# Kernel optimization log

Measured on AMD Instinct MI355X. Metric: run time of the kernel, lower is better.

The kernel has to match this reference:

```python
import jax, jax.numpy as jnp
import numpy as np

NUM_Q = 8
CODEBOOK_SIZE = 1024
DIM = 512
TEMP = 0.1


def _conv1d(x, w, b):
    # x: [B, C_in, T], w: [C_out, C_in, 3], padding 'same' (pad 1 each side)
    y = jax.lax.conv_general_dilated(
        x, w, window_strides=(1,), padding=((1, 1),),
        dimension_numbers=("NCH", "OIH", "NCH"))
    return y + b[None, :, None]


def _gelu(x):
    return jax.nn.gelu(x, approximate=False)  # torch default GELU is exact erf


def setup_inputs() -> dict:
    key = jax.random.key(0)
    ks = jax.random.split(key, 10)
    B, T = 8, 2048
    s = 0.05
    return {
        "x": jax.random.normal(ks[0], (B, T, 100), jnp.float32),
        "enc_w1": jax.random.normal(ks[1], (256, 100, 3), jnp.float32) * s,
        "enc_b1": jnp.zeros((256,), jnp.float32),
        "enc_w2": jax.random.normal(ks[2], (512, 256, 3), jnp.float32) * s,
        "enc_b2": jnp.zeros((512,), jnp.float32),
        "codebook": jax.random.normal(ks[3], (CODEBOOK_SIZE, DIM), jnp.float32),
        "dec_w1": jax.random.normal(ks[4], (256, 512, 3), jnp.float32) * s,
        "dec_b1": jnp.zeros((256,), jnp.float32),
        "dec_w2": jax.random.normal(ks[5], (100, 256, 3), jnp.float32) * s,
        "dec_b2": jnp.zeros((100,), jnp.float32),
    }


def reference(x, enc_w1, enc_b1, enc_w2, enc_b2, codebook,
              dec_w1, dec_b1, dec_w2, dec_b2):
    # ---- encoder: Conv1d(100->256)+GELU, Conv1d(256->512)+GELU ----
    h = jnp.transpose(x, (0, 2, 1))                      # [B, 100, T]
    h = _gelu(_conv1d(h, enc_w1, enc_b1))
    h = _gelu(_conv1d(h, enc_w2, enc_b2))
    z = jnp.transpose(h, (0, 2, 1))                      # [B, T, 512]

    # ---- residual VQ, 8 stages, shared euclidean codebook, stochastic sampling ----
    gkey = jax.random.key(42)
    c_sq = jnp.sum(codebook * codebook, axis=-1)         # [K]
    residual = z
    q_out = jnp.zeros_like(z)
    losses = []
    for i in range(NUM_Q):
        # negative squared euclidean distance [B, T, K]
        dist = -(jnp.sum(residual * residual, axis=-1, keepdims=True)
                 - 2.0 * jnp.einsum("btd,kd->btk", residual, codebook)
                 + c_sq)
        gumbel = jax.random.gumbel(jax.random.fold_in(gkey, i), dist.shape, dist.dtype)
        idx = jnp.argmax(dist / TEMP + gumbel, axis=-1)  # [B, T]
        q = codebook[idx]                                # gather [B, T, 512]
        # commitment loss (commitment_weight = 1.0)
        losses.append(jnp.mean((jax.lax.stop_gradient(q) - residual) ** 2))
        # straight-through quantize
        q_st = residual + jax.lax.stop_gradient(q - residual)
        q_out = q_out + q_st
        residual = residual - jax.lax.stop_gradient(q)
    commit_loss = jnp.mean(jnp.stack(losses))

    # ---- decoder: Conv1d(512->256)+GELU, Conv1d(256->100)+GELU ----
    h = jnp.transpose(q_out, (0, 2, 1))                  # [B, 512, T]
    h = _gelu(_conv1d(h, dec_w1, dec_b1))
    h = _gelu(_conv1d(h, dec_w2, dec_b2))
    y = jnp.transpose(h, (0, 2, 1))                      # [B, T, 100]

    return jnp.mean((x - y) ** 2) + commit_loss
```

## Files before the change

kernel.cpp:

```cpp
#include <hip/hip_runtime.h>
#include <cstdint>

namespace {

constexpr int kT = 2048;
constexpr int kTok = 16384;
constexpr int kD = 512;
constexpr int kK = 1024;

typedef __attribute__((ext_vector_type(8))) short short8;
typedef __attribute__((ext_vector_type(4))) float f32x4;

__device__ __forceinline__ float bf2f(uint16_t u) {
  union { uint32_t i; float f; } c; c.i = ((uint32_t)u) << 16; return c.f;
}
__device__ __forceinline__ uint16_t f2bf(float x) {
  union { float f; uint32_t i; } c; c.f = x;
  uint32_t lsb = (c.i >> 16) & 1u;
  return (uint16_t)((c.i + 0x7FFFu + lsb) >> 16);
}
__device__ __forceinline__ float gelu_f(float v) {
  return 0.5f * v * (1.0f + erff(v * 0.70710678118654752440f));
}
__device__ __forceinline__ uint32_t rotl32(uint32_t x, int r) {
  return (x << r) | (x >> (32 - r));
}

__device__ __forceinline__ void tf2x32(uint32_t k0, uint32_t k1,
                                       uint32_t x0, uint32_t x1,
                                       uint32_t& o0, uint32_t& o1) {
  const uint32_t k2 = k0 ^ k1 ^ 0x1BD11BDAu;
  x0 += k0; x1 += k1;
#define TF_R(r) { x0 += x1; x1 = rotl32(x1, (r)); x1 ^= x0; }
  TF_R(13) TF_R(15) TF_R(26) TF_R(6)
  x0 += k1; x1 += k2 + 1u;
  TF_R(17) TF_R(29) TF_R(16) TF_R(24)
  x0 += k2; x1 += k0 + 2u;
  TF_R(13) TF_R(15) TF_R(26) TF_R(6)
  x0 += k0; x1 += k1 + 3u;
  TF_R(17) TF_R(29) TF_R(16) TF_R(24)
  x0 += k1; x1 += k2 + 4u;
  TF_R(13) TF_R(15) TF_R(26) TF_R(6)
  x0 += k2; x1 += k0 + 5u;
#undef TF_R
  o0 = x0; o1 = x1;
}

__device__ __forceinline__ float gumbel_bits(uint32_t bits) {
  float f = __uint_as_float((bits >> 9) | 0x3f800000u) - 1.0f;
  const float tiny = 1.17549435e-38f;
  float u = fmaxf(tiny, f + tiny);
  return -__logf(-__logf(u));
}

__device__ __forceinline__ uint32_t pk_fp8x4(float f0, float f1, float f2, float f3) {
  int v = __builtin_amdgcn_cvt_pk_fp8_f32(f0, f1, 0, 0);
  v = __builtin_amdgcn_cvt_pk_fp8_f32(f2, f3, v, 1);
  return (uint32_t)v;
}

__global__ __launch_bounds__(256) void detect_kernel(const uint32_t* __restrict__ w,
                                                     uint32_t* __restrict__ flag) {
  __shared__ int red[256];
  int c = 0;
#pragma unroll
  for (int j = 0; j < 16; ++j) {
    uint32_t v = w[threadIdx.x * 16 + j];
    uint32_t e0 = (v >> 7) & 0xFFu;
    c += (e0 >= 100u && e0 <= 130u) ? 1 : 0;
  }
  red[threadIdx.x] = c;
  __syncthreads();
  for (int st = 128; st > 0; st >>= 1) {
    if (threadIdx.x < st) red[threadIdx.x] += red[threadIdx.x + st];
    __syncthreads();
  }
  if (threadIdx.x == 0) flag[0] = (red[0] > 2048) ? 1u : 0u;
}

__device__ __forceinline__ float load_flag(const void* src, size_t i, uint32_t fl) {
  return fl ? bf2f(((const uint16_t*)src)[i]) : ((const float*)src)[i];
}

__global__ __launch_bounds__(256) void prep_kernel(
    const void* x, const void* w1, const void* b1, const void* w2, const void* b2,
    const void* w3, const void* b3, const void* w4, const void* b4,
    uint16_t* __restrict__ xbf,
    uint16_t* __restrict__ W1, uint16_t* __restrict__ W2,
    uint16_t* __restrict__ W3, uint16_t* __restrict__ W4,
    float* __restrict__ eb1, float* __restrict__ eb2,
    float* __restrict__ db1, float* __restrict__ db2,
    const uint32_t* __restrict__ flag) {
  int gi = blockIdx.x * 256 + threadIdx.x;
  uint32_t fl = flag[0];
  if (gi < 2097152) {
    int tok = gi >> 7, ci = gi & 127;
    uint16_t v = 0;
    if (ci < 100) v = f2bf(load_flag(x, (size_t)tok * 100 + ci, fl));
    xbf[gi] = v;
    return;
  }
  int i = gi - 2097152;
  if (i < 98304) {
    int tap = i / 32768, rem = i % 32768;
    int co = rem >> 7, ci = rem & 127;
    uint16_t v = 0;
    if (ci < 100) v = f2bf(load_flag(w1, ((size_t)co * 100 + ci) * 3 + tap, fl));
    W1[i] = v;
  } else if (i < 491520) {
    int li = i - 98304;
    int tap = li / 131072, rem = li % 131072;
    int co = rem >> 8, ci = rem & 255;
    W2[li] = f2bf(load_flag(w2, ((size_t)co * 256 + ci) * 3 + tap, fl));
  } else if (i < 884736) {
    int li = i - 491520;
    int tap = li / 131072, rem = li % 131072;
    int co = rem >> 9, ci = rem & 511;
    W3[li] = f2bf(load_flag(w3, ((size_t)co * 512 + ci) * 3 + tap, fl));
  } else if (i < 983040) {
    int li = i - 884736;
    int tap = li / 32768, rem = li % 32768;
    int co = rem >> 8, ci = rem & 255;
    uint16_t v = 0;
    if (co < 100) v = f2bf(load_flag(w4, ((size_t)co * 256 + ci) * 3 + tap, fl));
    W4[li] = v;
  } else if (i < 983296) {
    eb1[i - 983040] = load_flag(b1, i - 983040, fl);
  } else if (i < 983808) {
    eb2[i - 983296] = load_flag(b2, i - 983296, fl);
  } else if (i < 984064) {
    db1[i - 983808] = load_flag(b3, i - 983808, fl);
  } else if (i < 984164) {
    db2[i - 984064] = load_flag(b4, i - 984064, fl);
  }
}

__global__ __launch_bounds__(512) void cb_prep_kernel(
    const void* __restrict__ src, float* __restrict__ cbf,
    uint8_t* __restrict__ cb8, float* __restrict__ c_sq,
    const uint32_t* __restrict__ flag) {
  __shared__ float red[8];
  const int row = blockIdx.x, t = threadIdx.x;
  const size_t i = (size_t)row * 512 + t;
  float f;
  if (flag[0]) f = bf2f(((const uint16_t*)src)[i]);
  else         f = ((const float*)src)[i];
  cbf[i] = f;
  {
    int g = t >> 6;
    int rem = t & 63;
    int half = rem >> 5;
    int quad = (rem & 31) >> 3;
    int j = t & 7;
    int off = g * 64 + quad * 16 + half * 8 + j;
    cb8[(size_t)row * 512 + off] =
        (uint8_t)(__builtin_amdgcn_cvt_pk_fp8_f32(f, f, 0, 0) & 0xFF);
  }
  float s = f * f;
  for (int off = 32; off > 0; off >>= 1) s += __shfl_down(s, off, 64);
  if ((t & 63) == 0) red[t >> 6] = s;
  __syncthreads();
  if (t == 0) {
    float tot = 0.f;
#pragma unroll
    for (int j = 0; j < 8; ++j) tot += red[j];
    c_sq[row] = tot;
  }
}

__global__ __launch_bounds__(512, 2) void gram_kernel(
    const float* __restrict__ cbf, float* __restrict__ gram) {
  constexpr int AST = 520;
  __shared__ uint16_t Ab[32 * AST];
  const int tid = threadIdx.x;
  const int w = tid >> 6;
  const int lane = tid & 63;
  const int quad = lane >> 4;
  const int col = lane & 15;
  const int bi = blockIdx.x >> 1;
  const int jb = blockIdx.x & 1;

  for (int m = tid; m < 32 * 128; m += 512) {
    int r = m >> 7, c4 = (m & 127) * 4;
    float4 v = *(const float4*)(cbf + (size_t)(bi * 32 + r) * 512 + c4);
    union { uint16_t u[4]; uint2 q; } o;
    o.u[0] = f2bf(v.x); o.u[1] = f2bf(v.y);
    o.u[2] = f2bf(v.z); o.u[3] = f2bf(v.w);
    *(uint2*)(Ab + r * AST + c4) = o.q;
  }
  __syncthreads();

  f32x4 acc[2][4];
#pragma unroll
  for (int mt = 0; mt < 2; ++mt)
#pragma unroll
    for (int nt = 0; nt < 4; ++nt) acc[mt][nt] = (f32x4){0.f, 0.f, 0.f, 0.f};

#pragma unroll 1
  for (int g = 0; g < 16; ++g) {
    short8 af0 = *(const short8*)(Ab + (size_t)col * AST + g * 32 + quad * 8);
    short8 af1 = *(const short8*)(Ab + (size_t)(16 + col) * AST + g * 32 + quad * 8);
#pragma unroll
    for (int nt = 0; nt < 4; ++nt) {
      const int j = jb * 512 + w * 64 + nt * 16 + col;
      const float* bp = cbf + (size_t)j * 512 + g * 32 + quad * 8;
      float4 b0 = *(const float4*)bp;
      float4 b1 = *(const float4*)(bp + 4);
      union { uint16_t u[8]; short8 s; } bf;
      bf.u[0] = f2bf(b0.x); bf.u[1] = f2bf(b0.y);
      bf.u[2] = f2bf(b0.z); bf.u[3] = f2bf(b0.w);
      bf.u[4] = f2bf(b1.x); bf.u[5] = f2bf(b1.y);
      bf.u[6] = f2bf(b1.z); bf.u[7] = f2bf(b1.w);
      acc[0][nt] = __builtin_amdgcn_mfma_f32_16x16x32_bf16(af0, bf.s, acc[0][nt], 0, 0, 0);
      acc[1][nt] = __builtin_amdgcn_mfma_f32_16x16x32_bf16(af1, bf.s, acc[1][nt], 0, 0, 0);
    }
  }
#pragma unroll
  for (int mt = 0; mt < 2; ++mt)
#pragma unroll
    for (int nt = 0; nt < 4; ++nt)
#pragma unroll
      for (int rg = 0; rg < 4; ++rg)
        gram[(size_t)(bi * 32 + mt * 16 + quad * 4 + rg) * 1024 +
             jb * 512 + w * 64 + nt * 16 + col] = acc[mt][nt][rg];
}

template <int TOK, int CIP, int COP, int CO_REAL, int OMODE>
__global__ __launch_bounds__(256, 2) void conv_mfma_kernel(
    const uint16_t* __restrict__ A, const uint16_t* __restrict__ W,
    const float* __restrict__ bias, uint16_t* __restrict__ outb,
    const void* __restrict__ xraw, const uint32_t* __restrict__ flag,
    float* __restrict__ partial) {
  constexpr int MT = TOK / 16;
  constexpr int AST = CIP + 8;
  __shared__ uint16_t As[(TOK + 2) * AST];
  __shared__ uint16_t Bs[128 * 72];
  __shared__ float red[256];

  const int tid = threadIdx.x;
  const int w = tid >> 6;
  const int lane = tid & 63;
  const int quad = lane >> 4;
  const int col = lane & 15;
  const int tok0 = blockIdx.x * TOK;
  const int t0 = tok0 & (kT - 1);

  constexpr int AV = (TOK + 2) * (CIP / 8);
  for (int m = tid; m < AV; m += 256) {
    int r = m / (CIP / 8), c8 = m % (CIP / 8);
    bool valid = !((r == 0 && t0 == 0) || (r == TOK + 1 && t0 == kT - TOK));
    uint4 v = {0, 0, 0, 0};
    if (valid) v = *(const uint4*)(A + (size_t)(tok0 - 1 + r) * CIP + c8 * 8);
    *(uint4*)(As + r * AST + c8 * 8) = v;
  }

  float part = 0.f;
#pragma unroll 1
  for (int chunk = 0; chunk < COP / 128; ++chunk) {
    f32x4 acc[MT][2];
#pragma unroll
    for (int mt = 0; mt < MT; ++mt)
#pragma unroll
      for (int nt = 0; nt < 2; ++nt) acc[mt][nt] = (f32x4){0.f, 0.f, 0.f, 0.f};

#pragma unroll 1
    for (int tap = 0; tap < 3; ++tap) {
#pragma unroll 1
      for (int kt = 0; kt < CIP / 64; ++kt) {
        __syncthreads();
#pragma unroll
        for (int it = 0; it < 4; ++it) {
          int m = it * 256 + tid;
          int rr = m >> 3, c8 = m & 7;
          *(uint4*)(Bs + rr * 72 + c8 * 8) =
              *(const uint4*)(W + ((size_t)tap * COP + chunk * 128 + rr) * CIP + kt * 64 + c8 * 8);
        }
        __syncthreads();
#pragma unroll
        for (int kk = 0; kk < 2; ++kk) {
          short8 bf0 = *(const short8*)(Bs + (w * 32 + col) * 72 + kk * 32 + quad * 8);
          short8 bf1 = *(const short8*)(Bs + (w * 32 + 16 + col) * 72 + kk * 32 + quad * 8);
#pragma unroll
          for (int mt = 0; mt < MT; ++mt) {
            short8 af = *(const short8*)(As + (mt * 16 + col + tap) * AST + kt * 64 + kk * 32 + quad * 8);
            acc[mt][0] = __builtin_amdgcn_mfma_f32_16x16x32_bf16(af, bf0, acc[mt][0], 0, 0, 0);
            acc[mt][1] = __builtin_amdgcn_mfma_f32_16x16x32_bf16(af, bf1, acc[mt][1], 0, 0, 0);
          }
        }
      }
    }
#pragma unroll
    for (int nt = 0; nt < 2; ++nt) {
      const int co = chunk * 128 + w * 32 + nt * 16 + col;
      const float bv = (OMODE == 1 && co >= CO_REAL) ? 0.f : bias[co];
#pragma unroll
      for (int mt = 0; mt < MT; ++mt) {
#pragma unroll
        for (int rg = 0; rg < 4; ++rg) {
          const int token = tok0 + mt * 16 + quad * 4 + rg;
          float g = gelu_f(acc[mt][nt][rg] + bv);
          if constexpr (OMODE == 0) {
            outb[(size_t)token * CO_REAL + co] = f2bf(g);
          } else {
            if (co < CO_REAL) {
              float xv = load_flag(xraw, (size_t)token * CO_REAL + co, flag[0]);
              float d = xv - g;
              part += d * d;
            }
          }
        }
      }
    }
  }
  if constexpr (OMODE == 1) {
    red[tid] = part;
    __syncthreads();
    for (int st = 128; st > 0; st >>= 1) {
      if (tid < st) red[tid] += red[tid + st];
      __syncthreads();
    }
    if (tid == 0) partial[blockIdx.x] = red[0];
  }
}

__global__ __launch_bounds__(512, 4) void vq_fused_kernel(
    const uint16_t* __restrict__ z,
    uint16_t* __restrict__ Aout,
    const uint8_t* __restrict__ cb8, const float* __restrict__ cbf,
    const float* __restrict__ csqG, const float* __restrict__ gram,
    float* __restrict__ cp) {
  constexpr int AST8 = 528;
  constexpr int AST16 = 520;
  __shared__ uint8_t  As8[32 * AST8];
  __shared__ uint16_t As16[32 * AST16];
  __shared__ float csqS[1024];
  __shared__ float dmaxW[32 * 8];
  __shared__ float thrS[32];
  __shared__ float wredV[32 * 8];
  __shared__ int   wredI[32 * 8];
  __shared__ int   idxS[32];
  __shared__ float credW[8];

  const int tid = threadIdx.x;
  const int w = tid >> 6;
  const int lane = tid & 63;
  const int quad = lane >> 4;
  const int col = lane & 15;
  const int blk = blockIdx.x;
  const int tokA = blk * 16;

  if (tid < 256) ((f32x4*)csqS)[tid] = ((const f32x4*)csqG)[tid];

#pragma unroll
  for (int it = 0; it < 4; ++it) {
    int m = it * 512 + tid;
    int r = m >> 6, c8 = m & 63;
    int tk = (r < 16) ? (tokA + r) : (8192 + tokA + r - 16);
    uint4 v = *(const uint4*)(z + (size_t)tk * 512 + c8 * 8);
    *(uint4*)(As16 + r * AST16 + c8 * 8) = v;
    const uint32_t* vp = (const uint32_t*)&v;
    float f[8];
#pragma unroll
    for (int q = 0; q < 4; ++q) {
      f[q * 2]     = bf2f((uint16_t)(vp[q] & 0xFFFFu));
      f[q * 2 + 1] = bf2f((uint16_t)(vp[q] >> 16));
    }
    uint2 pk;
    pk.x = pk_fp8x4(f[0], f[1], f[2], f[3]);
    pk.y = pk_fp8x4(f[4], f[5], f[6], f[7]);
    int ks = c8 >> 2, qd = c8 & 3;
    int off = (ks >> 1) * 64 + qd * 16 + (ks & 1) * 8;
    *(uint2*)(As8 + r * AST8 + off) = pk;
  }
  __syncthreads();

  const uint8_t* bb8 = cb8 + (size_t)(w * 128 + col) * 512 + (size_t)quad * 16;
  const int lr = tid >> 4;
  const int utok = (lr < 16) ? (tokA + lr) : (8192 + tokA + lr - 16);
  uint16_t* arow = As16 + lr * AST16;

  f32x4 acc[2][8];
#pragma unroll
  for (int mt = 0; mt < 2; ++mt)
#pragma unroll
    for (int nt = 0; nt < 8; ++nt) acc[mt][nt] = (f32x4){0.f, 0.f, 0.f, 0.f};

#pragma unroll 1
  for (int stage = 0; stage < 8; ++stage) {
    uint32_t key0, key1;
    tf2x32(0u, 42u, 0u, (uint32_t)stage, key0, key1);

    if (stage == 0) {
#pragma unroll 1
      for (int g = 0; g < 8; ++g) {
        ulong2 av0 = *(const ulong2*)(As8 + (size_t)(col) * AST8 + g * 64 + quad * 16);
        ulong2 av1 = *(const ulong2*)(As8 + (size_t)(16 + col) * AST8 + g * 64 + quad * 16);
#pragma unroll
        for (int nh = 0; nh < 2; ++nh) {
          ulong2 bfr[4];
#pragma unroll
          for (int j = 0; j < 4; ++j)
            bfr[j] = *(const ulong2*)(bb8 + (size_t)(nh * 4 + j) * 8192 + g * 64);
#pragma unroll
          for (int j = 0; j < 4; ++j) {
            acc[0][nh * 4 + j] = __builtin_amdgcn_mfma_f32_16x16x32_fp8_fp8(
                (long)av0.x, (long)bfr[j].x, acc[0][nh * 4 + j], 0, 0, 0);
            acc[0][nh * 4 + j] = __builtin_amdgcn_mfma_f32_16x16x32_fp8_fp8(
                (long)av0.y, (long)bfr[j].y, acc[0][nh * 4 + j], 0, 0, 0);
            acc[1][nh * 4 + j] = __builtin_amdgcn_mfma_f32_16x16x32_fp8_fp8(
                (long)av1.x, (long)bfr[j].x, acc[1][nh * 4 + j], 0, 0, 0);
            acc[1][nh * 4 + j] = __builtin_amdgcn_mfma_f32_16x16x32_fp8_fp8(
                (long)av1.y, (long)bfr[j].y, acc[1][nh * 4 + j], 0, 0, 0);
          }
        }
      }
    }

    float dmx[2][4];
#pragma unroll
    for (int mt = 0; mt < 2; ++mt)
#pragma unroll
      for (int rg = 0; rg < 4; ++rg) dmx[mt][rg] = -INFINITY;
#pragma unroll
    for (int nt = 0; nt < 8; ++nt) {
      const int code = w * 128 + nt * 16 + col;
      const float csqv = csqS[code];
#pragma unroll
      for (int mt = 0; mt < 2; ++mt)
#pragma unroll
        for (int rg = 0; rg < 4; ++rg)
          dmx[mt][rg] = fmaxf(dmx[mt][rg], acc[mt][nt][rg] * 2.f - csqv);
    }
#pragma unroll
    for (int mt = 0; mt < 2; ++mt)
#pragma unroll
      for (int rg = 0; rg < 4; ++rg) {
        float v = dmx[mt][rg];
#pragma unroll
        for (int m = 8; m >= 1; m >>= 1) v = fmaxf(v, __shfl_xor(v, m));
        if (col == 0) dmaxW[(mt * 16 + quad * 4 + rg) * 8 + w] = v;
      }
    __syncthreads();
    if (tid < 32) {
      float v = dmaxW[tid * 8];
#pragma unroll
      for (int j = 1; j < 8; ++j) v = fmaxf(v, dmaxW[tid * 8 + j]);
      thrS[tid] = v - 2.2f;
    }
    __syncthreads();

    float thr[2][4];
#pragma unroll
    for (int mt = 0; mt < 2; ++mt)
#pragma unroll
      for (int rg = 0; rg < 4; ++rg) thr[mt][rg] = thrS[mt * 16 + quad * 4 + rg];

    float bestV[2][4];
    int bestI[2][4];
#pragma unroll
    for (int mt = 0; mt < 2; ++mt)
#pragma unroll
      for (int rg = 0; rg < 4; ++rg) { bestV[mt][rg] = -INFINITY; bestI[mt][rg] = 0; }

#pragma unroll
    for (int nt = 0; nt < 8; ++nt) {
      const int code = w * 128 + nt * 16 + col;
      const float csqv = csqS[code];
#pragma unroll
      for (int rg = 0; rg < 4; ++rg) {
        float d0 = acc[0][nt][rg] * 2.f - csqv;
        float d1 = acc[1][nt][rg] * 2.f - csqv;
        bool c0 = d0 >= thr[0][rg];
        bool c1 = d1 >= thr[1][rg];
        if (c0 || c1) {
          const int row0 = quad * 4 + rg;
          const uint32_t n = (uint32_t)(tokA + row0) * 1024u + (uint32_t)code;
          uint32_t o0, o1;
          tf2x32(key0, key1, n, n + 8388608u, o0, o1);
          if (c0) {
            float s0 = d0 * 10.f + gumbel_bits(o0);
            if (s0 > bestV[0][rg]) { bestV[0][rg] = s0; bestI[0][rg] = code; }
          }
          if (c1) {
            float s1 = d1 * 10.f + gumbel_bits(o1);
            if (s1 > bestV[1][rg]) { bestV[1][rg] = s1; bestI[1][rg] = code; }
          }
        }
      }
    }

#pragma unroll
    for (int mt = 0; mt < 2; ++mt)
#pragma unroll
      for (int rg = 0; rg < 4; ++rg) {
        float v = bestV[mt][rg];
        int i = bestI[mt][rg];
#pragma unroll
        for (int m = 8; m >= 1; m >>= 1) {
          float vo = __shfl_xor(v, m);
          int io = __shfl_xor(i, m);
          if (vo > v || (vo == v && io < i)) { v = vo; i = io; }
        }
        if (col == 0) {
          const int row = mt * 16 + quad * 4 + rg;
          wredV[row * 8 + w] = v;
          wredI[row * 8 + w] = i;
        }
      }
    __syncthreads();
    if (tid < 32) {
      float v = wredV[tid * 8];
      int i = wredI[tid * 8];
#pragma unroll
      for (int j = 1; j < 8; ++j) {
        float vo = wredV[tid * 8 + j];
        int io = wredI[tid * 8 + j];
        if (vo > v || (vo == v && io < i)) { v = vo; i = io; }
      }
      idxS[tid] = i;
    }
    __syncthreads();

    const int code = idxS[lr];
    const float* qrow = cbf + (size_t)code * 512;
    float s = 0.f;
#pragma unroll 1
    for (int it = 0; it < 8; ++it) {
      const int d = (tid & 15) * 4 + it * 64;
      float4 q = *(const float4*)(qrow + d);
      uint2 rp = *(const uint2*)(arow + d);
      union { uint16_t u[4]; uint2 v; } ri, ro;
      ri.v = rp;
      float r0 = bf2f(ri.u[0]), r1 = bf2f(ri.u[1]);
      float r2 = bf2f(ri.u[2]), r3 = bf2f(ri.u[3]);
      float d0 = q.x - r0, d1 = q.y - r1, d2 = q.z - r2, d3 = q.w - r3;
      s += d0 * d0 + d1 * d1 + d2 * d2 + d3 * d3;
      ro.u[0] = f2bf(r0 - q.x); ro.u[1] = f2bf(r1 - q.y);
      ro.u[2] = f2bf(r2 - q.z); ro.u[3] = f2bf(r3 - q.w);
      if (stage == 7) {
        uint2 zp = *(const uint2*)(z + (size_t)utok * 512 + d);
        union { uint16_t u[4]; uint2 v; } zi, od;
        zi.v = zp;
        od.u[0] = f2bf(bf2f(zi.u[0]) - bf2f(ro.u[0]));
        od.u[1] = f2bf(bf2f(zi.u[1]) - bf2f(ro.u[1]));
        od.u[2] = f2bf(bf2f(zi.u[2]) - bf2f(ro.u[2]));
        od.u[3] = f2bf(bf2f(zi.u[3]) - bf2f(ro.u[3]));
        *(uint2*)(Aout + (size_t)utok * 512 + d) = od.v;
      } else {
        *(uint2*)(arow + d) = ro.v;
      }
    }

    if (stage < 7) {
#define DGRP(MT, RG) { \
      const float* gp_ = gram + (size_t)idxS[(MT) * 16 + quad * 4 + (RG)] * 1024 \
                         + w * 128 + col; \
      float g0_ = gp_[0],  g1_ = gp_[16], g2_ = gp_[32], g3_ = gp_[48]; \
      float g4_ = gp_[64], g5_ = gp_[80], g6_ = gp_[96], g7_ = gp_[112]; \
      acc[MT][0][RG] -= g0_; acc[MT][1][RG] -= g1_; \
      acc[MT][2][RG] -= g2_; acc[MT][3][RG] -= g3_; \
      acc[MT][4][RG] -= g4_; acc[MT][5][RG] -= g5_; \
      acc[MT][6][RG] -= g6_; acc[MT][7][RG] -= g7_; }
      DGRP(0, 0) DGRP(0, 1)
      __builtin_amdgcn_sched_barrier(0);
      DGRP(0, 2) DGRP(0, 3)
      __builtin_amdgcn_sched_barrier(0);
      DGRP(1, 0) DGRP(1, 1)
      __builtin_amdgcn_sched_barrier(0);
      DGRP(1, 2) DGRP(1, 3)
#undef DGRP
    }

#pragma unroll
    for (int m = 32; m >= 1; m >>= 1) s += __shfl_xor(s, m);
    if (lane == 0) credW[w] = s;
    __syncthreads();
    if (tid == 0) {
      float tot = 0.f;
#pragma unroll
      for (int j = 0; j < 8; ++j) tot += credW[j];
      cp[stage * 512 + blk] = tot;
    }
  }
}

__global__ __launch_bounds__(256) void finalize_kernel(
    const float* __restrict__ cp, int ncp, const float* __restrict__ mp, int nmp,
    uint32_t* __restrict__ out) {
  __shared__ double sd[256];
  const int tid = threadIdx.x;
  double s = 0.0, sm = 0.0;
  for (int m = tid; m < ncp; m += 256) s += (double)cp[m];
  for (int m = tid; m < nmp; m += 256) sm += (double)mp[m];
  sd[tid] = s;
  __syncthreads();
  for (int st = 128; st > 0; st >>= 1) {
    if (tid < st) sd[tid] += sd[tid + st];
    __syncthreads();
  }
  double commit_total = sd[0];
  __syncthreads();
  sd[tid] = sm;
  __syncthreads();
  for (int st = 128; st > 0; st >>= 1) {
    if (tid < st) sd[tid] += sd[tid + st];
    __syncthreads();
  }
  if (tid == 0) {
    double commit = commit_total / (16384.0 * 512.0) / 8.0;
    double mse = sd[0] / (16384.0 * 100.0);
    float res = (float)(mse + commit);
    uint32_t fb = __float_as_uint(res);
    uint32_t lsb = (fb >> 16) & 1u;
    uint32_t hb = (fb + 0x7FFFu + lsb) >> 16;
    out[0] = (hb << 16) | hb;
  }
}

}

extern "C" void kernel_launch(void* const* d_in, const int* in_sizes, int n_in,
                              void* d_out, int out_size, void* d_ws, size_t ws_size,
                              hipStream_t stream) {
  char* ws = (char*)d_ws;
  uint16_t* z     = (uint16_t*)(ws + 0);
  uint16_t* h     = (uint16_t*)(ws + 16777216);
  uint16_t* rbf   = (uint16_t*)(ws + 25165824);
  uint16_t* xbf   = (uint16_t*)(ws + 41943040);
  uint8_t*  cb8   = (uint8_t*) (ws + 46137344);
  float*    cbf   = (float*)   (ws + 47185920);
  uint16_t* Wenc1 = (uint16_t*)(ws + 49283072);
  uint16_t* Wenc2 = (uint16_t*)(ws + 49479680);
  uint16_t* Wdec1 = (uint16_t*)(ws + 50266112);
  uint16_t* Wdec2 = (uint16_t*)(ws + 51052544);
  float*    eb1   = (float*)   (ws + 51249152);
  float*    eb2   = (float*)   (ws + 51250176);
  float*    db1   = (float*)   (ws + 51252224);
  float*    db2   = (float*)   (ws + 51253248);
  float*    csqG  = (float*)   (ws + 51253760);
  float*    cp    = (float*)   (ws + 51257856);
  float*    mp    = (float*)   (ws + 51274240);
  uint32_t* flag  = (uint32_t*)(ws + 51276288);
  float*    gramT = (float*)   (ws + 41943040);

  detect_kernel<<<1, 256, 0, stream>>>((const uint32_t*)d_in[0], flag);

  prep_kernel<<<(2097152 + 984164 + 255) / 256, 256, 0, stream>>>(
      d_in[0], d_in[1], d_in[2], d_in[3], d_in[4], d_in[6], d_in[7], d_in[8], d_in[9],
      xbf, Wenc1, Wenc2, Wdec1, Wdec2, eb1, eb2, db1, db2, flag);
  cb_prep_kernel<<<1024, 512, 0, stream>>>(d_in[5], cbf, cb8, csqG, flag);

  conv_mfma_kernel<32, 128, 256, 256, 0><<<512, 256, 0, stream>>>(
      xbf, Wenc1, eb1, h, nullptr, flag, nullptr);
  gram_kernel<<<64, 512, 0, stream>>>(cbf, gramT);
  conv_mfma_kernel<32, 256, 512, 512, 0><<<512, 256, 0, stream>>>(
      h, Wenc2, eb2, z, nullptr, flag, nullptr);

  vq_fused_kernel<<<512, 512, 0, stream>>>(z, rbf, cb8, cbf, csqG, gramT, cp);

  conv_mfma_kernel<32, 512, 256, 256, 0><<<512, 256, 0, stream>>>(
      rbf, Wdec1, db1, h, nullptr, flag, nullptr);
  conv_mfma_kernel<32, 256, 128, 100, 1><<<512, 256, 0, stream>>>(
      h, Wdec2, db2, nullptr, d_in[0], flag, mp);

  finalize_kernel<<<1, 256, 0, stream>>>(cp, 8 * 512, mp, 512, (uint32_t*)d_out);
}
```

Baseline: 432.8 us.

## Use LDS atomics for per-row reductions and permute gram layout for vector loads

Replaces the two-phase per-row max and argmax reductions (per-warp shared arrays plus a serial 32-thread pass and an extra barrier each) with order-preserving uint atomicMax into double-buffered LDS slots, packing score and inverted index into one 64-bit key. This removes two __syncthreads and the serial reduction per stage. It also permutes the gram matrix layout so each lane's eight per-code gram values are contiguous and load as two float4s instead of eight strided scalars. The Gumbel branch becomes a wave-uniform ballot test, which lets whole waves skip RNG work together but makes every lane evaluate when any lane qualifies.

After: 429.4 us. About the same (-0.8%).

```diff
diff --git a/kernel.cpp b/kernel.cpp
--- a/kernel.cpp
+++ b/kernel.cpp
@@ -24,6 +24,15 @@
 }
 __device__ __forceinline__ uint32_t rotl32(uint32_t x, int r) {
   return (x << r) | (x >> (32 - r));
+}
+
+__device__ __forceinline__ uint32_t ford(float f) {
+  uint32_t b = __float_as_uint(f);
+  return (b & 0x80000000u) ? ~b : (b | 0x80000000u);
+}
+__device__ __forceinline__ float funord(uint32_t u) {
+  uint32_t b = (u & 0x80000000u) ? (u ^ 0x80000000u) : ~u;
+  return __uint_as_float(b);
 }
 
 __device__ __forceinline__ void tf2x32(uint32_t k0, uint32_t k1,
@@ -220,9 +229,12 @@
 #pragma unroll
     for (int nt = 0; nt < 4; ++nt)
 #pragma unroll
-      for (int rg = 0; rg < 4; ++rg)
-        gram[(size_t)(bi * 32 + mt * 16 + quad * 4 + rg) * 1024 +
-             jb * 512 + w * 64 + nt * 16 + col] = acc[mt][nt][rg];
+      for (int rg = 0; rg < 4; ++rg) {
+        const int i_ = bi * 32 + mt * 16 + quad * 4 + rg;
+        const int j_ = jb * 512 + w * 64 + nt * 16 + col;
+        gram[(size_t)i_ * 1024 + (j_ >> 7) * 128 + (j_ & 15) * 8 + ((j_ >> 4) & 7)] =
+            acc[mt][nt][rg];
+      }
 }
 
 template <int TOK, int CIP, int COP, int CO_REAL, int OMODE>
@@ -334,11 +346,8 @@
   __shared__ uint8_t  As8[32 * AST8];
   __shared__ uint16_t As16[32 * AST16];
   __shared__ float csqS[1024];
-  __shared__ float dmaxW[32 * 8];
-  __shared__ float thrS[32];
-  __shared__ float wredV[32 * 8];
-  __shared__ int   wredI[32 * 8];
-  __shared__ int   idxS[32];
+  __shared__ uint32_t dmaxA[2][32];
+  __shared__ unsigned long long bestA[2][32];
   __shared__ float credW[8];
 
   const int tid = threadIdx.x;
@@ -350,6 +359,7 @@
   const int tokA = blk * 16;
 
   if (tid < 256) ((f32x4*)csqS)[tid] = ((const f32x4*)csqG)[tid];
+  if (tid < 32) { dmaxA[0][tid] = 0u; bestA[0][tid] = 0ull; }
 
 #pragma unroll
   for (int it = 0; it < 4; ++it) {
@@ -387,6 +397,7 @@
 
 #pragma unroll 1
   for (int stage = 0; stage < 8; ++stage) {
+    const int p = stage & 1;
     uint32_t key0, key1;
     tf2x32(0u, 42u, 0u, (uint32_t)stage, key0, key1);
 
@@ -438,22 +449,16 @@
         float v = dmx[mt][rg];
 #pragma unroll
         for (int m = 8; m >= 1; m >>= 1) v = fmaxf(v, __shfl_xor(v, m));
-        if (col == 0) dmaxW[(mt * 16 + quad * 4 + rg) * 8 + w] = v;
+        if (col == 0) atomicMax(&dmaxA[p][mt * 16 + quad * 4 + rg], ford(v));
       }
     __syncthreads();
-    if (tid < 32) {
-      float v = dmaxW[tid * 8];
-#pragma unroll
-      for (int j = 1; j < 8; ++j) v = fmaxf(v, dmaxW[tid * 8 + j]);
-      thrS[tid] = v - 2.2f;
-    }
-    __syncthreads();
 
     float thr[2][4];
 #pragma unroll
     for (int mt = 0; mt < 2; ++mt)
 #pragma unroll
-      for (int rg = 0; rg < 4; ++rg) thr[mt][rg] = thrS[mt * 16 + quad * 4 + rg];
+      for (int rg = 0; rg < 4; ++rg)
+        thr[mt][rg] = funord(dmaxA[p][mt * 16 + quad * 4 + rg]) - 2.2f;
 
     float bestV[2][4];
     int bestI[2][4];
@@ -472,7 +477,7 @@
         float d1 = acc[1][nt][rg] * 2.f - csqv;
         bool c0 = d0 >= thr[0][rg];
         bool c1 = d1 >= thr[1][rg];
-        if (c0 || c1) {
+        if (__ballot(c0 || c1)) {
           const int row0 = quad * 4 + rg;
           const uint32_t n = (uint32_t)(tokA + row0) * 1024u + (uint32_t)code;
           uint32_t o0, o1;
@@ -502,26 +507,15 @@
           if (vo > v || (vo == v && io < i)) { v = vo; i = io; }
         }
         if (col == 0) {
-          const int row = mt * 16 + quad * 4 + rg;
-          wredV[row * 8 + w] = v;
-          wredI[row * 8 + w] = i;
+          unsigned long long pk = ((unsigned long long)ford(v) << 16) |
+                                  (unsigned long long)(1023 - i);
+          atomicMax(&bestA[p][mt * 16 + quad * 4 + rg], pk);
         }
       }
     __syncthreads();
-    if (tid < 32) {
-      float v = wredV[tid * 8];
-      int i = wredI[tid * 8];
-#pragma unroll
-      for (int j = 1; j < 8; ++j) {
-        float vo = wredV[tid * 8 + j];
-        int io = wredI[tid * 8 + j];
-        if (vo > v || (vo == v && io < i)) { v = vo; i = io; }
-      }
-      idxS[tid] = i;
-    }
-    __syncthreads();
-
-    const int code = idxS[lr];
+
+    const int code = 1023 - (int)(bestA[p][lr] & 0xFFFFu);
+    if (tid < 32) { dmaxA[p ^ 1][tid] = 0u; bestA[p ^ 1][tid] = 0ull; }
     const float* qrow = cbf + (size_t)code * 512;
     float s = 0.f;
 #pragma unroll 1
@@ -553,14 +547,15 @@
 
     if (stage < 7) {
 #define DGRP(MT, RG) { \
-      const float* gp_ = gram + (size_t)idxS[(MT) * 16 + quad * 4 + (RG)] * 1024 \
-                         + w * 128 + col; \
-      float g0_ = gp_[0],  g1_ = gp_[16], g2_ = gp_[32], g3_ = gp_[48]; \
-      float g4_ = gp_[64], g5_ = gp_[80], g6_ = gp_[96], g7_ = gp_[112]; \
-      acc[MT][0][RG] -= g0_; acc[MT][1][RG] -= g1_; \
-      acc[MT][2][RG] -= g2_; acc[MT][3][RG] -= g3_; \
-      acc[MT][4][RG] -= g4_; acc[MT][5][RG] -= g5_; \
-      acc[MT][6][RG] -= g6_; acc[MT][7][RG] -= g7_; }
+      const int row_ = (MT) * 16 + quad * 4 + (RG); \
+      const int c_ = 1023 - (int)(bestA[p][row_] & 0xFFFFu); \
+      const float* gp_ = gram + (size_t)c_ * 1024 + w * 128 + col * 8; \
+      float4 ga_ = *(const float4*)gp_; \
+      float4 gb_ = *(const float4*)(gp_ + 4); \
+      acc[MT][0][RG] -= ga_.x; acc[MT][1][RG] -= ga_.y; \
+      acc[MT][2][RG] -= ga_.z; acc[MT][3][RG] -= ga_.w; \
+      acc[MT][4][RG] -= gb_.x; acc[MT][5][RG] -= gb_.y; \
+      acc[MT][6][RG] -= gb_.z; acc[MT][7][RG] -= gb_.w; }
       DGRP(0, 0) DGRP(0, 1)
       __builtin_amdgcn_sched_barrier(0);
       DGRP(0, 2) DGRP(0, 3)
```
